# Performance work log

Hardware: AMD Instinct MI355X
Metric: run time of the kernel (lower is better)

The kernel has to match this reference:

```python
import jax, jax.numpy as jnp
import numpy as np

TEMP = 20.0
ATT_WT = 0.5
EPS = 1e-12


def _l2n(x, axis):
    return x / jnp.maximum(jnp.linalg.norm(x, axis=axis, keepdims=True), EPS)


def _conv2d(x, w, b, pad, dil):
    y = jax.lax.conv_general_dilated(
        x, w, window_strides=(1, 1), padding=[(pad, pad), (pad, pad)],
        rhs_dilation=(dil, dil), dimension_numbers=("NCHW", "OIHW", "NCHW"))
    return y + b[None, :, None, None]


def _maxpool3(x):
    return jax.lax.reduce_window(x, -jnp.inf, jax.lax.max,
                                 (1, 1, 3, 3), (1, 1, 3, 3), "VALID")


def setup_inputs() -> dict:
    key = jax.random.key(0)
    ks = jax.random.split(key, 8)
    L, B, C, h, w = 9, 4, 512, 32, 32
    sc = 0.05
    return {
        "fq_feats": jax.random.normal(ks[0], (L, B, C, h, w), jnp.float32),
        "fs_feats": jax.random.normal(ks[1], (L, B, C, h, w), jnp.float32),
        "f_q": jax.random.normal(ks[2], (B, C, h, w), jnp.float32),
        "f_s": jax.random.normal(ks[3], (B, C, h, w), jnp.float32),
        "w1": jax.random.normal(ks[4], (256, 1024, 3, 3), jnp.float32) * sc,
        "b1": jnp.zeros((256,), jnp.float32),
        "w2": jax.random.normal(ks[5], (256, 256, 3, 3), jnp.float32) * sc,
        "b2": jnp.zeros((256,), jnp.float32),
        "w3": jax.random.normal(ks[6], (1, 256, 3, 3), jnp.float32) * sc,
        "b3": jnp.zeros((1,), jnp.float32),
    }


def reference(fq_feats, fs_feats, f_q, f_s, w1, b1, w2, b2, w3, b3):
    B, C, h, w = f_q.shape
    # per-level cosine correlation volumes: normalize over channel dim
    fq_n = _l2n(fq_feats, axis=2)  # [L,B,C,h,w]
    fs_n = _l2n(fs_feats, axis=2)
    corr = jnp.einsum("lbcxy,lbcuv->lbxyuv", fq_n, fs_n)  # [L,B,h,w,h,w]
    # MatchNet corr_forward: ReLU'd volumes fused across hyperpixel levels,
    # temperature softmax over support positions, aggregate support values v=f_s
    corr = jax.nn.relu(corr).mean(axis=0)                 # [B,h,w,h,w]
    attn = jax.nn.softmax(corr.reshape(B, h * w, h * w) * TEMP, axis=-1)
    att_fq = jnp.einsum("bqs,bcs->bcq", attn, f_s.reshape(B, C, h * w))
    att_fq = att_fq.reshape(B, C, h, w)
    fq = _l2n(f_q, axis=1) + _l2n(att_fq, axis=1) * ATT_WT
    # AttentionBranch (Dropout2d is identity at inference)
    comp = jnp.concatenate((f_q, f_s), axis=1)            # [B,1024,h,w]
    x = jax.nn.relu(_conv2d(comp, w1, b1, pad=2, dil=2))  # [B,256,32,32]
    x = _conv2d(x, w2, b2, pad=0, dil=1)                  # [B,256,30,30]
    x = _maxpool3(x)                                      # [B,256,10,10]
    x = _conv2d(x, w3, b3, pad=0, dil=1)                  # [B,1,8,8]
    weight = x.mean(axis=(2, 3)).squeeze()[None]          # [1,B]
    return fq, att_fq, weight
```

## Files before the change

kernel.cpp:

```cpp
#include <hip/hip_runtime.h>
#include <hip/hip_bf16.h>

#define DI __device__ __forceinline__

typedef short bf16x8_t __attribute__((ext_vector_type(8)));
typedef _Float16 f16x8_t __attribute__((ext_vector_type(8)));
typedef float f32x4_t __attribute__((ext_vector_type(4)));

DI unsigned short f2bf(float f) {
    unsigned u = __float_as_uint(f);
    u += 0x7fffu + ((u >> 16) & 1u);
    return (unsigned short)(u >> 16);
}
DI float bfu2f(unsigned short u) { return __uint_as_float(((unsigned)u) << 16); }
DI unsigned short f2h(float f) {
    _Float16 h = (_Float16)f;
    unsigned short u;
    __builtin_memcpy(&u, &h, 2);
    return u;
}
DI float h2f(unsigned short u) {
    _Float16 h;
    __builtin_memcpy(&h, &u, 2);
    return (float)h;
}

__global__ __launch_bounds__(256) void k_prep(const float* __restrict__ fqf,
                                              const float* __restrict__ fsf,
                                              unsigned short* __restrict__ fqb,
                                              unsigned short* __restrict__ fsb,
                                              float* __restrict__ rq,
                                              float* __restrict__ rs) {
    __shared__ float T[128 * 33];
    const int pt = blockIdx.x;
    const int lb = blockIdx.y;
    const int tz = blockIdx.z;
    const float* src = (tz ? fsf : fqf) + (size_t)lb * 524288 + pt * 128;
    unsigned short* dst = (tz ? fsb : fqb) + (((size_t)(lb * 8 + pt)) << 16);
    float* rdst = (tz ? rs : rq) + lb * 1024 + pt * 128;
    const int t = threadIdx.x;

    const int m0 = t >> 2, m1 = 64 + (t >> 2);
    const int q0 = (t & 3) ^ ((m0 >> 2) & 3);
    const int q1 = (t & 3) ^ ((m1 >> 2) & 3);
    float ssq0 = 0.f, ssq1 = 0.f;

    const int brow = t >> 5;
    float4 v[4];
    auto load = [&](int ks) {
#pragma unroll
        for (int j = 0; j < 4; ++j) {
            int f = t + (j << 8);
            int row = f >> 5;
            int m4 = (f & 31) << 2;
            v[j] = *(const float4*)(src + (((size_t)(ks * 32 + row)) << 10) + m4);
        }
    };

    load(0);
    for (int ks = 0; ks < 16; ++ks) {
        __syncthreads();
#pragma unroll
        for (int j = 0; j < 4; ++j) {
            int f = t + (j << 8);
            int row = f >> 5;
            int m4 = (f & 31) << 2;
            T[(m4 + 0) * 33 + row] = v[j].x;
            T[(m4 + 1) * 33 + row] = v[j].y;
            T[(m4 + 2) * 33 + row] = v[j].z;
            T[(m4 + 3) * 33 + row] = v[j].w;
        }
        __syncthreads();
        if (ks < 15) load(ks + 1);
        {
            const float* Tp = &T[m0 * 33 + q0 * 8];
            float f0 = Tp[0], f1 = Tp[1], f2 = Tp[2], f3 = Tp[3];
            float f4 = Tp[4], f5 = Tp[5], f6 = Tp[6], f7 = Tp[7];
            ssq0 += f0 * f0 + f1 * f1 + f2 * f2 + f3 * f3 +
                    f4 * f4 + f5 * f5 + f6 * f6 + f7 * f7;
            uint4 r4;
            r4.x = (unsigned)f2h(f0) | ((unsigned)f2h(f1) << 16);
            r4.y = (unsigned)f2h(f2) | ((unsigned)f2h(f3) << 16);
            r4.z = (unsigned)f2h(f4) | ((unsigned)f2h(f5) << 16);
            r4.w = (unsigned)f2h(f6) | ((unsigned)f2h(f7) << 16);
            *(uint4*)(dst + ((size_t)ks << 12) + ((size_t)t << 3)) = r4;
        }
        {
            const float* Tp = &T[m1 * 33 + q1 * 8];
            float f0 = Tp[0], f1 = Tp[1], f2 = Tp[2], f3 = Tp[3];
            float f4 = Tp[4], f5 = Tp[5], f6 = Tp[6], f7 = Tp[7];
            ssq1 += f0 * f0 + f1 * f1 + f2 * f2 + f3 * f3 +
                    f4 * f4 + f5 * f5 + f6 * f6 + f7 * f7;
            uint4 r4;
            r4.x = (unsigned)f2h(f0) | ((unsigned)f2h(f1) << 16);
            r4.y = (unsigned)f2h(f2) | ((unsigned)f2h(f3) << 16);
            r4.z = (unsigned)f2h(f4) | ((unsigned)f2h(f5) << 16);
            r4.w = (unsigned)f2h(f6) | ((unsigned)f2h(f7) << 16);
            *(uint4*)(dst + ((size_t)ks << 12) + ((size_t)(t + 256) << 3)) = r4;
        }
    }
    ssq0 += __shfl_xor(ssq0, 1); ssq0 += __shfl_xor(ssq0, 2);
    ssq1 += __shfl_xor(ssq1, 1); ssq1 += __shfl_xor(ssq1, 2);
    if ((t & 3) == 0) {
        rdst[m0] = 1.f / fmaxf(sqrtf(ssq0), 1e-12f);
        rdst[m1] = 1.f / fmaxf(sqrtf(ssq1), 1e-12f);
    }
}

__global__ __launch_bounds__(256) void k_corr2(const unsigned short* __restrict__ fqb,
                                               const unsigned short* __restrict__ fsb,
                                               const float* __restrict__ rq,
                                               const float* __restrict__ rs,
                                               unsigned short* __restrict__ P01) {
    __shared__ __align__(16) char L[2][16384];
    const int id = blockIdx.x;
    const int z = id & 7, local = id >> 3;
    const int b = z >> 1, lg = z & 1;
    const int qt = local >> 3, st = local & 7;
    const int q0 = qt * 128, s0 = st * 128;
    const int t = threadIdx.x;
    const int w = t >> 6, lane = t & 63;
    const int wrow = w >> 1, wcol = w & 1;
    const int quad = lane >> 4, m16 = lane & 15;
    const int nsteps = (5 - lg) << 4;

    f32x4_t zero4 = {0.f, 0.f, 0.f, 0.f};
    f32x4_t master[4][4], lvl[4][4];
#pragma unroll
    for (int i = 0; i < 4; ++i)
#pragma unroll
        for (int j = 0; j < 4; ++j) { master[i][j] = zero4; lvl[i][j] = zero4; }

    auto stage = [&](int step, int buf) {
        int g = step >> 4, ks = step & 15;
        int lb = (lg + 2 * g) * 4 + b;
        const unsigned short* Ab = fqb + ((((size_t)lb * 8 + qt) * 16 + ks) << 12);
        const unsigned short* Bb = fsb + ((((size_t)lb * 8 + st) * 16 + ks) << 12);
#pragma unroll
        for (int i = 0; i < 4; ++i) {
            int idx0 = i * 256 + w * 64;
            int idx = idx0 + lane;
            const unsigned short* srcp = (idx0 < 512)
                ? (Ab + ((size_t)idx << 3))
                : (Bb + ((size_t)(idx - 512) << 3));
            __builtin_amdgcn_global_load_lds(
                (const __attribute__((address_space(1))) void*)srcp,
                (__attribute__((address_space(3))) void*)(&L[buf][0] + idx0 * 16),
                16, 0, 0);
        }
    };

    stage(0, 0);
    for (int step = 0; step < nsteps; ++step) {
        const int buf = step & 1;
        __syncthreads();
        if (step < nsteps - 1) stage(step + 1, buf ^ 1);
        const char* base = &L[buf][0];
        f16x8_t af[4], bfr[4];
#pragma unroll
        for (int i = 0; i < 4; ++i) {
            int m = wrow * 64 + i * 16 + m16;
            int sa = quad ^ ((m >> 2) & 3);
            af[i] = *(const f16x8_t*)(base + m * 64 + sa * 16);
            int n = wcol * 64 + i * 16 + m16;
            int sb = quad ^ ((n >> 2) & 3);
            bfr[i] = *(const f16x8_t*)(base + 8192 + n * 64 + sb * 16);
        }
#pragma unroll
        for (int mi = 0; mi < 4; ++mi)
#pragma unroll
            for (int ni = 0; ni < 4; ++ni)
                lvl[mi][ni] = __builtin_amdgcn_mfma_f32_16x16x32_f16(
                    af[mi], bfr[ni], lvl[mi][ni], 0, 0, 0);

        if ((step & 15) == 15) {
            int lb = (lg + 2 * (step >> 4)) * 4 + b;
            const float* rqb = rq + lb * 1024 + q0 + wrow * 64;
            const float* rsb = rs + lb * 1024 + s0 + wcol * 64;
            float rq4[4][4], rsv[4];
#pragma unroll
            for (int mi = 0; mi < 4; ++mi) {
                float4 vv = *(const float4*)(rqb + mi * 16 + quad * 4);
                rq4[mi][0] = vv.x; rq4[mi][1] = vv.y; rq4[mi][2] = vv.z; rq4[mi][3] = vv.w;
            }
#pragma unroll
            for (int ni = 0; ni < 4; ++ni) rsv[ni] = rsb[ni * 16 + m16];
#pragma unroll
            for (int mi = 0; mi < 4; ++mi)
#pragma unroll
                for (int ni = 0; ni < 4; ++ni) {
#pragma unroll
                    for (int e = 0; e < 4; ++e)
                        master[mi][ni][e] += fmaxf(lvl[mi][ni][e] * rq4[mi][e] * rsv[ni], 0.f);
                    lvl[mi][ni] = zero4;
                }
        }
    }

#pragma unroll
    for (int mi = 0; mi < 4; ++mi)
#pragma unroll
        for (int e = 0; e < 4; ++e) {
            int q = q0 + wrow * 64 + mi * 16 + quad * 4 + e;
            unsigned short* cp = P01 + ((((size_t)(lg * 4 + b)) * 1024 + q) << 10)
                                 + s0 + wcol * 64 + m16;
#pragma unroll
            for (int ni = 0; ni < 4; ++ni)
                cp[ni * 16] = f2h(master[mi][ni][e]);
        }
}

__global__ __launch_bounds__(256) void k_softmax(const unsigned short* __restrict__ P01,
                                                 unsigned short* __restrict__ attn) {
    __shared__ float red[8];
    const int row = blockIdx.x;
    const int b = row >> 10, q = row & 1023;
    const int t = threadIdx.x;
    const unsigned short* p0 = P01 + (((size_t)b << 20) + ((size_t)q << 10)) + t * 4;
    const unsigned short* p1 = p0 + ((size_t)4 << 20);
    uint2 a0 = *(const uint2*)p0;
    uint2 a1 = *(const uint2*)p1;
    const float SC = 20.f / 9.f;
    float v0 = (h2f(a0.x & 0xffff) + h2f(a1.x & 0xffff)) * SC;
    float v1 = (h2f(a0.x >> 16)    + h2f(a1.x >> 16)) * SC;
    float v2 = (h2f(a0.y & 0xffff) + h2f(a1.y & 0xffff)) * SC;
    float v3 = (h2f(a0.y >> 16)    + h2f(a1.y >> 16)) * SC;
    float m = fmaxf(fmaxf(v0, v1), fmaxf(v2, v3));
#pragma unroll
    for (int off = 32; off >= 1; off >>= 1) m = fmaxf(m, __shfl_down(m, off));
    const int wid = t >> 6, lane = t & 63;
    if (lane == 0) red[wid] = m;
    __syncthreads();
    m = fmaxf(fmaxf(red[0], red[1]), fmaxf(red[2], red[3]));
    float e0 = __expf(v0 - m), e1 = __expf(v1 - m);
    float e2 = __expf(v2 - m), e3 = __expf(v3 - m);
    float s = e0 + e1 + e2 + e3;
#pragma unroll
    for (int off = 32; off >= 1; off >>= 1) s += __shfl_down(s, off);
    if (lane == 0) red[4 + wid] = s;
    __syncthreads();
    s = red[4] + red[5] + red[6] + red[7];
    float inv = 1.f / s;
    unsigned short* o = attn + (size_t)((b * 32 + (t >> 3)) * 1024 + q) * 36 + (t & 7) * 4;
    uint2 r;
    r.x = (unsigned)f2h(e0 * inv) | ((unsigned)f2h(e1 * inv) << 16);
    r.y = (unsigned)f2h(e2 * inv) | ((unsigned)f2h(e3 * inv) << 16);
    *(uint2*)o = r;
}

__global__ __launch_bounds__(256) void k_fspack(const float* __restrict__ fsi,
                                                unsigned short* __restrict__ fsp) {
    int id = blockIdx.x * 256 + threadIdx.x;
    int c = id & 511, sb = (id >> 9) & 31, b = id >> 14;
    const float4* src = (const float4*)(fsi + (((size_t)(b * 512 + c)) << 10) + sb * 32);
    unsigned short* dst = fsp + (size_t)((b * 32 + sb) * 512 + c) * 36;
#pragma unroll
    for (int j = 0; j < 8; ++j) {
        float4 v = src[j];
        uint2 r;
        r.x = (unsigned)f2h(v.x) | ((unsigned)f2h(v.y) << 16);
        r.y = (unsigned)f2h(v.z) | ((unsigned)f2h(v.w) << 16);
        *(uint2*)(dst + j * 4) = r;
    }
}

__global__ __launch_bounds__(256) void k_attfqm(const unsigned short* __restrict__ fsp,
                                                const unsigned short* __restrict__ attn,
                                                float* __restrict__ attfq) {
    __shared__ __align__(16) char L[2][14336];
    const int q0 = blockIdx.x * 128;
    const int c0 = blockIdx.y * 64;
    const int b  = blockIdx.z;
    const int t = threadIdx.x;
    const int w = t >> 6, lane = t & 63;
    const int quad = lane >> 4, m16 = lane & 15;

    f32x4_t acc[4][2];
#pragma unroll
    for (int i = 0; i < 4; ++i)
#pragma unroll
        for (int j = 0; j < 2; ++j) acc[i][j] = (f32x4_t){0.f, 0.f, 0.f, 0.f};

    auto stage = [&](int sb, int buf) {
        const char* sa = (const char*)(fsp + (size_t)((b * 32 + sb) * 512 + c0) * 36);
        const char* sbp = (const char*)(attn + (size_t)((b * 32 + sb) * 1024 + q0) * 36);
#pragma unroll
        for (int i = 0; i < 4; ++i) {
            int idx0 = i * 256 + w * 64;
            if (idx0 < 896) {
                int idx = idx0 + lane;
                const char* src = (idx < 288) ? (sa + idx * 16) : (sbp + (idx - 288) * 16);
                __builtin_amdgcn_global_load_lds(
                    (const __attribute__((address_space(1))) void*)src,
                    (__attribute__((address_space(3))) void*)(&L[buf][0] + idx0 * 16),
                    16, 0, 0);
            }
        }
    };

    stage(0, 0);
    for (int sb = 0; sb < 32; ++sb) {
        const int buf = sb & 1;
        __syncthreads();
        if (sb < 31) stage(sb + 1, buf ^ 1);
        const char* base = &L[buf][0];
        f16x8_t af[4], bfr[2];
#pragma unroll
        for (int i = 0; i < 4; ++i) {
            const char* ap = base + (size_t)(i * 16 + m16) * 72 + quad * 16;
            union { unsigned long long d[2]; f16x8_t v; } u;
            u.d[0] = *(const unsigned long long*)ap;
            u.d[1] = *(const unsigned long long*)(ap + 8);
            af[i] = u.v;
        }
#pragma unroll
        for (int ni = 0; ni < 2; ++ni) {
            const char* bp = base + 4608 + (size_t)(w * 32 + ni * 16 + m16) * 72 + quad * 16;
            union { unsigned long long d[2]; f16x8_t v; } u;
            u.d[0] = *(const unsigned long long*)bp;
            u.d[1] = *(const unsigned long long*)(bp + 8);
            bfr[ni] = u.v;
        }
#pragma unroll
        for (int mi = 0; mi < 4; ++mi)
#pragma unroll
            for (int ni = 0; ni < 2; ++ni)
                acc[mi][ni] = __builtin_amdgcn_mfma_f32_16x16x32_f16(
                    af[mi], bfr[ni], acc[mi][ni], 0, 0, 0);
    }

#pragma unroll
    for (int mi = 0; mi < 4; ++mi)
#pragma unroll
        for (int e = 0; e < 4; ++e) {
            int c = c0 + mi * 16 + quad * 4 + e;
            float* rowp = attfq + (((size_t)(b * 512 + c)) << 10) + q0 + w * 32 + m16;
#pragma unroll
            for (int ni = 0; ni < 2; ++ni)
                rowp[ni * 16] = acc[mi][ni][e];
        }
}

__global__ __launch_bounds__(256) void k_out(const float* __restrict__ fqi,
                                             const float* __restrict__ attfq,
                                             float* __restrict__ out) {
    __shared__ float redq[256], reda[256];
    __shared__ float rnq[64], rna[64];
    const int b = blockIdx.y;
    const int p0 = blockIdx.x * 64;
    const int t = threadIdx.x;
    const int pl = t & 63, cg = t >> 6;
    const int pos = p0 + pl;
    const float* qp = fqi + (((size_t)b) << 19) + pos;
    const float* ap = attfq + (((size_t)b) << 19) + pos;
    float sq = 0.f, sa = 0.f;
    for (int c = cg * 128; c < cg * 128 + 128; ++c) {
        float q = qp[(size_t)c << 10];
        float a = ap[(size_t)c << 10];
        sq += q * q;
        sa += a * a;
    }
    redq[t] = sq; reda[t] = sa;
    __syncthreads();
    if (t < 64) {
        float q = redq[t] + redq[t + 64] + redq[t + 128] + redq[t + 192];
        float a = reda[t] + reda[t + 64] + reda[t + 128] + reda[t + 192];
        rnq[t] = 1.f / fmaxf(sqrtf(q), 1e-12f);
        rna[t] = 1.f / fmaxf(sqrtf(a), 1e-12f);
    }
    __syncthreads();
    const float RQ = rnq[pl], RA = 0.5f * rna[pl];
    float* o1 = out + (((size_t)b) << 19) + pos;
    float* o2 = o1 + 2097152;
    for (int c = cg * 128; c < cg * 128 + 128; ++c) {
        float q = qp[(size_t)c << 10];
        float a = ap[(size_t)c << 10];
        o1[(size_t)c << 10] = q * RQ + a * RA;
        o2[(size_t)c << 10] = a;
    }
}

__global__ __launch_bounds__(256) void k_w1pack(const float* __restrict__ w1,
                                                unsigned short* __restrict__ w1p) {
    int pid = blockIdx.x * 256 + threadIdx.x;
    int oc = pid >> 10, ic = pid & 1023;
    const float* src = w1 + (size_t)pid * 9;
    float f[9];
#pragma unroll
    for (int tp = 0; tp < 9; ++tp) f[tp] = src[tp];
    int s = ic >> 5, j = ic & 31;
#pragma unroll
    for (int tp = 0; tp < 9; ++tp) {
        size_t row = ((size_t)(tp * 32 + s) * 256 + oc) * 40;
        w1p[row + j] = f2bf(f[tp]);
        if (j < 8) w1p[row + 32 + j] = 0;
    }
}

__global__ __launch_bounds__(256) void k_conv1m(const float* __restrict__ fqi,
                                                const float* __restrict__ fsi,
                                                const unsigned short* __restrict__ w1p,
                                                float* __restrict__ P) {
    __shared__ __align__(16) char As[2][20480];
    __shared__ __align__(16) char Bs[2][4096];
    const int p0 = blockIdx.x * 64;
    const int b = blockIdx.y;
    const int tap = blockIdx.z;
    const int dy = 2 * (tap / 3) - 2;
    const int dx = 2 * (tap % 3) - 2;
    const int t = threadIdx.x;
    const int w = t >> 6, lane = t & 63;
    const int quad = lane >> 4, m16 = lane & 15;
    const int bn = t & 63, kg = t >> 6;
    const int e0 = p0 + bn;
    const bool valid = ((unsigned)((e0 >> 5) + dy) < 32u) &&
                       ((unsigned)((e0 & 31) + dx) < 32u);
    const int cidx = min(max(e0 + dy * 32 + dx, 0), 1023);
    const int bchunk = (bn * 4 + (kg ^ (bn & 3))) * 16;

    f32x4_t acc[4][4];
#pragma unroll
    for (int i = 0; i < 4; ++i)
#pragma unroll
        for (int j = 0; j < 4; ++j) acc[i][j] = (f32x4_t){0.f, 0.f, 0.f, 0.f};

    auto stageA = [&](int s, int buf) {
        const char* src = (const char*)(w1p + (size_t)(tap * 32 + s) * 10240);
#pragma unroll
        for (int i = 0; i < 5; ++i) {
            int idx = i * 4 + w;
            __builtin_amdgcn_global_load_lds(
                (const __attribute__((address_space(1))) void*)(src + idx * 1024 + lane * 16),
                (__attribute__((address_space(3))) void*)(&As[buf][0] + idx * 1024),
                16, 0, 0);
        }
    };
    auto stageB = [&](int s, int buf) {
        int ch = s * 32 + kg * 8;
        const float* plane = (ch < 512)
            ? (fqi + (((size_t)(b * 512 + ch)) << 10))
            : (fsi + (((size_t)(b * 512 + ch - 512)) << 10));
        float f[8];
#pragma unroll
        for (int j = 0; j < 8; ++j) {
            float v = plane[((size_t)j << 10) + cidx];
            f[j] = valid ? v : 0.f;
        }
        uint4 r4;
        r4.x = (unsigned)f2bf(f[0]) | ((unsigned)f2bf(f[1]) << 16);
        r4.y = (unsigned)f2bf(f[2]) | ((unsigned)f2bf(f[3]) << 16);
        r4.z = (unsigned)f2bf(f[4]) | ((unsigned)f2bf(f[5]) << 16);
        r4.w = (unsigned)f2bf(f[6]) | ((unsigned)f2bf(f[7]) << 16);
        *(uint4*)(&Bs[buf][bchunk]) = r4;
    };

    stageA(0, 0);
    stageB(0, 0);

    for (int s = 0; s < 32; ++s) {
        const int buf = s & 1;
        __syncthreads();
        if (s < 31) {
            stageA(s + 1, buf ^ 1);
            stageB(s + 1, buf ^ 1);
        }
        bf16x8_t af[4], bfr[4];
#pragma unroll
        for (int i = 0; i < 4; ++i) {
            af[i] = *(const bf16x8_t*)(&As[buf][0] + (size_t)(w * 64 + i * 16 + m16) * 80 + quad * 16);
            int nn = i * 16 + m16;
            bfr[i] = *(const bf16x8_t*)(&Bs[buf][0] + (nn * 4 + (quad ^ (nn & 3))) * 16);
        }
#pragma unroll
        for (int mi = 0; mi < 4; ++mi)
#pragma unroll
            for (int ni = 0; ni < 4; ++ni)
                acc[mi][ni] = __builtin_amdgcn_mfma_f32_16x16x32_bf16(
                    af[mi], bfr[ni], acc[mi][ni], 0, 0, 0);
    }

    float* Pb = P + (((size_t)(tap * 4 + b)) << 18) + p0;
#pragma unroll
    for (int mi = 0; mi < 4; ++mi)
#pragma unroll
        for (int e = 0; e < 4; ++e) {
            int oc = w * 64 + mi * 16 + quad * 4 + e;
            float* row = Pb + (size_t)oc * 1024 + m16;
#pragma unroll
            for (int ni = 0; ni < 4; ++ni)
                row[ni * 16] = acc[mi][ni][e];
        }
}

__global__ __launch_bounds__(256) void k_c1comb(const float* __restrict__ P,
                                                const float* __restrict__ b1,
                                                unsigned short* __restrict__ x1) {
    int id = blockIdx.x * 256 + threadIdx.x;
    int oc = (id >> 8) & 255;
    const float4* P4 = (const float4*)P;
    float bb = b1[oc];
    float4 a = P4[id];
    a.x += bb; a.y += bb; a.z += bb; a.w += bb;
#pragma unroll
    for (int tp = 1; tp < 9; ++tp) {
        float4 v = P4[id + tp * 262144];
        a.x += v.x; a.y += v.y; a.z += v.z; a.w += v.w;
    }
    float o0 = fmaxf(a.x, 0.f);
    float o1 = fmaxf(a.y, 0.f);
    float o2 = fmaxf(a.z, 0.f);
    float o3 = fmaxf(a.w, 0.f);
    uint2 r;
    r.x = (unsigned)f2bf(o0) | ((unsigned)f2bf(o1) << 16);
    r.y = (unsigned)f2bf(o2) | ((unsigned)f2bf(o3) << 16);
    ((uint2*)x1)[id] = r;
}

__global__ __launch_bounds__(256) void k_w2pack(const float* __restrict__ w2,
                                                unsigned short* __restrict__ w2p) {
    int pid = blockIdx.x * 256 + threadIdx.x;
    int oc = pid >> 8, ic = pid & 255;
    const float* src = w2 + (size_t)pid * 9;
    float f[9];
#pragma unroll
    for (int tp = 0; tp < 9; ++tp) f[tp] = src[tp];
    int s = ic >> 5, j = ic & 31;
#pragma unroll
    for (int tp = 0; tp < 9; ++tp) {
        size_t row = ((size_t)(tp * 8 + s) * 256 + oc) * 40;
        w2p[row + j] = f2bf(f[tp]);
        if (j < 8) w2p[row + 32 + j] = 0;
    }
}

__global__ __launch_bounds__(256) void k_conv2m(const unsigned short* __restrict__ x1,
                                                const unsigned short* __restrict__ w2p,
                                                float* __restrict__ P2) {
    __shared__ __align__(16) char As[2][20480];
    __shared__ __align__(16) char Bs[2][4096];
    const int p0 = blockIdx.x * 64;
    const int b = blockIdx.y;
    const int tap = blockIdx.z;
    const int t = threadIdx.x;
    const int w = t >> 6, lane = t & 63;
    const int quad = lane >> 4, m16 = lane & 15;
    const int bn = t & 63, kg = t >> 6;
    const int e0 = p0 + bn;
    const int cidx = min(e0 + (tap / 3) * 32 + (tap % 3), 1023);
    const int bchunk = (bn * 4 + (kg ^ (bn & 3))) * 16;

    f32x4_t acc[4][4];
#pragma unroll
    for (int i = 0; i < 4; ++i)
#pragma unroll
        for (int j = 0; j < 4; ++j) acc[i][j] = (f32x4_t){0.f, 0.f, 0.f, 0.f};

    auto stageA = [&](int s, int buf) {
        const char* src = (const char*)(w2p + (size_t)(tap * 8 + s) * 10240);
#pragma unroll
        for (int i = 0; i < 5; ++i) {
            int idx = i * 4 + w;
            __builtin_amdgcn_global_load_lds(
                (const __attribute__((address_space(1))) void*)(src + idx * 1024 + lane * 16),
                (__attribute__((address_space(3))) void*)(&As[buf][0] + idx * 1024),
                16, 0, 0);
        }
    };
    auto stageB = [&](int s, int buf) {
        int ch = s * 32 + kg * 8;
        const unsigned short* plane = x1 + (((size_t)(b * 256 + ch)) << 10);
        unsigned short u[8];
#pragma unroll
        for (int j = 0; j < 8; ++j) u[j] = plane[((size_t)j << 10) + cidx];
        uint4 r4;
        r4.x = (unsigned)u[0] | ((unsigned)u[1] << 16);
        r4.y = (unsigned)u[2] | ((unsigned)u[3] << 16);
        r4.z = (unsigned)u[4] | ((unsigned)u[5] << 16);
        r4.w = (unsigned)u[6] | ((unsigned)u[7] << 16);
        *(uint4*)(&Bs[buf][bchunk]) = r4;
    };

    stageA(0, 0);
    stageB(0, 0);

    for (int s = 0; s < 8; ++s) {
        const int buf = s & 1;
        __syncthreads();
        if (s < 7) {
            stageA(s + 1, buf ^ 1);
            stageB(s + 1, buf ^ 1);
        }
        bf16x8_t af[4], bfr[4];
#pragma unroll
        for (int i = 0; i < 4; ++i) {
            af[i] = *(const bf16x8_t*)(&As[buf][0] + (size_t)(w * 64 + i * 16 + m16) * 80 + quad * 16);
            int nn = i * 16 + m16;
            bfr[i] = *(const bf16x8_t*)(&Bs[buf][0] + (nn * 4 + (quad ^ (nn & 3))) * 16);
        }
#pragma unroll
        for (int mi = 0; mi < 4; ++mi)
#pragma unroll
            for (int ni = 0; ni < 4; ++ni)
                acc[mi][ni] = __builtin_amdgcn_mfma_f32_16x16x32_bf16(
                    af[mi], bfr[ni], acc[mi][ni], 0, 0, 0);
    }

    float* Pb = P2 + (((size_t)(tap * 4 + b)) << 18) + p0;
#pragma unroll
    for (int mi = 0; mi < 4; ++mi)
#pragma unroll
        for (int e = 0; e < 4; ++e) {
            int oc = w * 64 + mi * 16 + quad * 4 + e;
            float* row = Pb + (size_t)oc * 1024 + m16;
#pragma unroll
            for (int ni = 0; ni < 4; ++ni)
                row[ni * 16] = acc[mi][ni][e];
        }
}

__global__ __launch_bounds__(256) void k_c2pool(const float* __restrict__ P2,
                                                const float* __restrict__ b2,
                                                float* __restrict__ xp) {
    int id = blockIdx.x * 256 + threadIdx.x;
    int px = id % 10;
    int tmp = id / 10;
    int py = tmp % 10;
    int ch = tmp / 10;
    int b = ch >> 8, oc = ch & 255;
    float bb = b2[oc];
    float m = -3.4e38f;
#pragma unroll
    for (int dy = 0; dy < 3; ++dy)
#pragma unroll
        for (int dx = 0; dx < 3; ++dx) {
            int pos = (3 * py + dy) * 32 + 3 * px + dx;
            float v = bb;
#pragma unroll
            for (int tp = 0; tp < 9; ++tp)
                v += P2[(((size_t)(tp * 4 + b)) << 18) + (size_t)oc * 1024 + pos];
            m = fmaxf(m, v);
        }
    xp[id] = m;
}

__global__ __launch_bounds__(256) void k_conv3(const float* __restrict__ xp,
                                               const float* __restrict__ w3,
                                               const float* __restrict__ b3,
                                               float* __restrict__ out) {
    __shared__ float s[256];
    int b = blockIdx.x, t = threadIdx.x;
    int pos = t & 63, qi = t >> 6;
    int y = pos >> 3, x = pos & 7;
    float acc = 0.f;
    for (int ic = qi * 64; ic < qi * 64 + 64; ++ic) {
        const float* ip = xp + ((size_t)(b * 256 + ic)) * 100 + y * 10 + x;
#pragma unroll
        for (int kh = 0; kh < 3; ++kh)
#pragma unroll
            for (int kw = 0; kw < 3; ++kw)
                acc = fmaf(w3[ic * 9 + kh * 3 + kw], ip[kh * 10 + kw], acc);
    }
    s[t] = acc;
    __syncthreads();
    if (t < 64) {
        float v = s[t] + s[t + 64] + s[t + 128] + s[t + 192];
#pragma unroll
        for (int off = 32; off >= 1; off >>= 1) v += __shfl_down(v, off);
        if (t == 0) out[4194304 + b] = v * (1.f / 64.f) + b3[0];
    }
}

extern "C" void kernel_launch(void* const* d_in, const int* in_sizes, int n_in,
                              void* d_out, int out_size, void* d_ws, size_t ws_size,
                              hipStream_t stream) {
    (void)in_sizes; (void)n_in; (void)out_size; (void)ws_size;
    const float* fqf = (const float*)d_in[0];
    const float* fsf = (const float*)d_in[1];
    const float* fqi = (const float*)d_in[2];
    const float* fsi = (const float*)d_in[3];
    const float* w1  = (const float*)d_in[4];
    const float* b1  = (const float*)d_in[5];
    const float* w2  = (const float*)d_in[6];
    const float* b2  = (const float*)d_in[7];
    const float* w3  = (const float*)d_in[8];
    const float* b3  = (const float*)d_in[9];
    float* out = (float*)d_out;

    float* W = (float*)d_ws;
    unsigned short* P01u = (unsigned short*)W;
    float* attfq = W;
    unsigned short* attn = (unsigned short*)(W + 4194304);
    unsigned short* w1p  = (unsigned short*)(W + 4194304);
    float* rq = W + 5668864;
    float* rs = W + 5705728;
    unsigned short* w2p  = (unsigned short*)(W + 4194304);
    unsigned short* fsp = (unsigned short*)(W + 6553600);
    unsigned short* x1 = (unsigned short*)(W + 7733248);
    float* xp = W + 8257536;
    unsigned short* fqb = (unsigned short*)(W + 8359936);
    float* P9 = W + 8359936;
    unsigned short* fsb = (unsigned short*)(W + 17797120);

    hipLaunchKernelGGL(k_w1pack,  dim3(1024),      dim3(256), 0, stream, w1, w1p);
    hipLaunchKernelGGL(k_conv1m,  dim3(16, 4, 9),  dim3(256), 0, stream, fqi, fsi, w1p, P9);
    hipLaunchKernelGGL(k_c1comb,  dim3(1024),      dim3(256), 0, stream, P9, b1, x1);
    hipLaunchKernelGGL(k_fspack,  dim3(256),       dim3(256), 0, stream, fsi, fsp);
    hipLaunchKernelGGL(k_prep,    dim3(8, 36, 2),  dim3(256), 0, stream, fqf, fsf, fqb, fsb, rq, rs);
    hipLaunchKernelGGL(k_corr2,   dim3(512),       dim3(256), 0, stream, fqb, fsb, rq, rs, P01u);
    hipLaunchKernelGGL(k_softmax, dim3(4096),      dim3(256), 0, stream, P01u, attn);
    hipLaunchKernelGGL(k_attfqm,  dim3(8, 8, 4),   dim3(256), 0, stream, fsp, attn, attfq);
    hipLaunchKernelGGL(k_out,     dim3(16, 4),     dim3(256), 0, stream, fqi, attfq, out);
    hipLaunchKernelGGL(k_w2pack,  dim3(256),       dim3(256), 0, stream, w2, w2p);
    hipLaunchKernelGGL(k_conv2m,  dim3(16, 4, 9),  dim3(256), 0, stream, x1, w2p, P9);
    hipLaunchKernelGGL(k_c2pool,  dim3(400),       dim3(256), 0, stream, P9, b2, xp);
    hipLaunchKernelGGL(k_conv3,   dim3(4),         dim3(256), 0, stream, xp, w3, b3, out);
}
```

Baseline: 450.9 us.

## Split prep over channel groups with partial norms, double-buffer LDS, widen k_out grid

k_prep now splits the 512-channel reduction into four groups per block, which quadruples the grid. Each group writes partial sums of squares, and a new k_rfold kernel combines them into reciprocal norms. The transpose tile in LDS is double-buffered, so one barrier per step covers both the write and the read. k_out uses 16 positions per block instead of 64, giving a 4x larger grid. This adds parallelism to the memory-bound kernels at the cost of one extra launch and less coalescing in k_out, since only 16 contiguous floats are read per row.

```diff
diff --git a/kernel.cpp b/kernel.cpp
--- a/kernel.cpp
+++ b/kernel.cpp
@@ -29,15 +29,16 @@
                                               const float* __restrict__ fsf,
                                               unsigned short* __restrict__ fqb,
                                               unsigned short* __restrict__ fsb,
-                                              float* __restrict__ rq,
-                                              float* __restrict__ rs) {
-    __shared__ float T[128 * 33];
+                                              float* __restrict__ rpart) {
+    __shared__ float T[2][128 * 33];
     const int pt = blockIdx.x;
     const int lb = blockIdx.y;
-    const int tz = blockIdx.z;
+    const int zz = blockIdx.z;
+    const int tz = zz >> 2, kg = zz & 3;
+    const int ks0 = kg * 4;
     const float* src = (tz ? fsf : fqf) + (size_t)lb * 524288 + pt * 128;
     unsigned short* dst = (tz ? fsb : fqb) + (((size_t)(lb * 8 + pt)) << 16);
-    float* rdst = (tz ? rs : rq) + lb * 1024 + pt * 128;
+    float* rdst = rpart + (size_t)tz * 147456 + (size_t)kg * 36864 + lb * 1024 + pt * 128;
     const int t = threadIdx.x;
 
     const int m0 = t >> 2, m1 = 64 + (t >> 2);
@@ -45,7 +46,6 @@
     const int q1 = (t & 3) ^ ((m1 >> 2) & 3);
     float ssq0 = 0.f, ssq1 = 0.f;
 
-    const int brow = t >> 5;
     float4 v[4];
     auto load = [&](int ks) {
 #pragma unroll
@@ -56,24 +56,29 @@
             v[j] = *(const float4*)(src + (((size_t)(ks * 32 + row)) << 10) + m4);
         }
     };
-
-    load(0);
-    for (int ks = 0; ks < 16; ++ks) {
-        __syncthreads();
+    auto writeT = [&](int buf) {
 #pragma unroll
         for (int j = 0; j < 4; ++j) {
             int f = t + (j << 8);
             int row = f >> 5;
             int m4 = (f & 31) << 2;
-            T[(m4 + 0) * 33 + row] = v[j].x;
-            T[(m4 + 1) * 33 + row] = v[j].y;
-            T[(m4 + 2) * 33 + row] = v[j].z;
-            T[(m4 + 3) * 33 + row] = v[j].w;
-        }
+            float* Tb = &T[buf][0];
+            Tb[(m4 + 0) * 33 + row] = v[j].x;
+            Tb[(m4 + 1) * 33 + row] = v[j].y;
+            Tb[(m4 + 2) * 33 + row] = v[j].z;
+            Tb[(m4 + 3) * 33 + row] = v[j].w;
+        }
+    };
+
+    load(ks0);
+    writeT(0);
+    for (int s = 0; s < 4; ++s) {
         __syncthreads();
-        if (ks < 15) load(ks + 1);
+        if (s < 3) load(ks0 + s + 1);
+        const int ks = ks0 + s;
+        const float* Tb = &T[s & 1][0];
         {
-            const float* Tp = &T[m0 * 33 + q0 * 8];
+            const float* Tp = Tb + m0 * 33 + q0 * 8;
             float f0 = Tp[0], f1 = Tp[1], f2 = Tp[2], f3 = Tp[3];
             float f4 = Tp[4], f5 = Tp[5], f6 = Tp[6], f7 = Tp[7];
             ssq0 += f0 * f0 + f1 * f1 + f2 * f2 + f3 * f3 +
@@ -86,7 +91,7 @@
             *(uint4*)(dst + ((size_t)ks << 12) + ((size_t)t << 3)) = r4;
         }
         {
-            const float* Tp = &T[m1 * 33 + q1 * 8];
+            const float* Tp = Tb + m1 * 33 + q1 * 8;
             float f0 = Tp[0], f1 = Tp[1], f2 = Tp[2], f3 = Tp[3];
             float f4 = Tp[4], f5 = Tp[5], f6 = Tp[6], f7 = Tp[7];
             ssq1 += f0 * f0 + f1 * f1 + f2 * f2 + f3 * f3 +
@@ -98,13 +103,24 @@
             r4.w = (unsigned)f2h(f6) | ((unsigned)f2h(f7) << 16);
             *(uint4*)(dst + ((size_t)ks << 12) + ((size_t)(t + 256) << 3)) = r4;
         }
+        if (s < 3) writeT((s + 1) & 1);
     }
     ssq0 += __shfl_xor(ssq0, 1); ssq0 += __shfl_xor(ssq0, 2);
     ssq1 += __shfl_xor(ssq1, 1); ssq1 += __shfl_xor(ssq1, 2);
     if ((t & 3) == 0) {
-        rdst[m0] = 1.f / fmaxf(sqrtf(ssq0), 1e-12f);
-        rdst[m1] = 1.f / fmaxf(sqrtf(ssq1), 1e-12f);
-    }
+        rdst[m0] = ssq0;
+        rdst[m1] = ssq1;
+    }
+}
+
+__global__ __launch_bounds__(256) void k_rfold(const float* __restrict__ rpart,
+                                               float* __restrict__ rout) {
+    int id = blockIdx.x * 256 + threadIdx.x;
+    int tz = id >= 36864;
+    int i = id - (tz ? 36864 : 0);
+    const float* p = rpart + (size_t)tz * 147456 + i;
+    float s = p[0] + p[36864] + p[73728] + p[110592];
+    rout[id] = 1.f / fmaxf(sqrtf(s), 1e-12f);
 }
 
 __global__ __launch_bounds__(256) void k_corr2(const unsigned short* __restrict__ fqb,
@@ -345,16 +361,16 @@
                                              const float* __restrict__ attfq,
                                              float* __restrict__ out) {
     __shared__ float redq[256], reda[256];
-    __shared__ float rnq[64], rna[64];
+    __shared__ float rnq[16], rna[16];
     const int b = blockIdx.y;
-    const int p0 = blockIdx.x * 64;
+    const int p0 = blockIdx.x * 16;
     const int t = threadIdx.x;
-    const int pl = t & 63, cg = t >> 6;
+    const int pl = t & 15, cg = t >> 4;
     const int pos = p0 + pl;
     const float* qp = fqi + (((size_t)b) << 19) + pos;
     const float* ap = attfq + (((size_t)b) << 19) + pos;
     float sq = 0.f, sa = 0.f;
-    for (int c = cg * 128; c < cg * 128 + 128; ++c) {
+    for (int c = cg * 32; c < cg * 32 + 32; ++c) {
         float q = qp[(size_t)c << 10];
         float a = ap[(size_t)c << 10];
         sq += q * q;
@@ -362,17 +378,18 @@
     }
     redq[t] = sq; reda[t] = sa;
     __syncthreads();
-    if (t < 64) {
-        float q = redq[t] + redq[t + 64] + redq[t + 128] + redq[t + 192];
-        float a = reda[t] + reda[t + 64] + reda[t + 128] + reda[t + 192];
+    if (t < 16) {
+        float q = 0.f, a = 0.f;
+#pragma unroll
+        for (int j = 0; j < 16; ++j) { q += redq[t + j * 16]; a += reda[t + j * 16]; }
         rnq[t] = 1.f / fmaxf(sqrtf(q), 1e-12f);
-        rna[t] = 1.f / fmaxf(sqrtf(a), 1e-12f);
+        rna[t] = 0.5f / fmaxf(sqrtf(a), 1e-12f);
     }
     __syncthreads();
-    const float RQ = rnq[pl], RA = 0.5f * rna[pl];
+    const float RQ = rnq[pl], RA = rna[pl];
     float* o1 = out + (((size_t)b) << 19) + pos;
     float* o2 = o1 + 2097152;
-    for (int c = cg * 128; c < cg * 128 + 128; ++c) {
+    for (int c = cg * 32; c < cg * 32 + 32; ++c) {
         float q = qp[(size_t)c << 10];
         float a = ap[(size_t)c << 10];
         o1[(size_t)c << 10] = q * RQ + a * RA;
@@ -691,8 +708,9 @@
     float* attfq = W;
     unsigned short* attn = (unsigned short*)(W + 4194304);
     unsigned short* w1p  = (unsigned short*)(W + 4194304);
-    float* rq = W + 5668864;
-    float* rs = W + 5705728;
+    float* rpart = W + 5668864;
+    float* rq = W + 5963776;
+    float* rs = W + 6000640;
     unsigned short* w2p  = (unsigned short*)(W + 4194304);
     unsigned short* fsp = (unsigned short*)(W + 6553600);
     unsigned short* x1 = (unsigned short*)(W + 7733248);
@@ -705,11 +723,12 @@
     hipLaunchKernelGGL(k_conv1m,  dim3(16, 4, 9),  dim3(256), 0, stream, fqi, fsi, w1p, P9);
     hipLaunchKernelGGL(k_c1comb,  dim3(1024),      dim3(256), 0, stream, P9, b1, x1);
     hipLaunchKernelGGL(k_fspack,  dim3(256),       dim3(256), 0, stream, fsi, fsp);
-    hipLaunchKernelGGL(k_prep,    dim3(8, 36, 2),  dim3(256), 0, stream, fqf, fsf, fqb, fsb, rq, rs);
+    hipLaunchKernelGGL(k_prep,    dim3(8, 36, 8),  dim3(256), 0, stream, fqf, fsf, fqb, fsb, rpart);
+    hipLaunchKernelGGL(k_rfold,   dim3(288),       dim3(256), 0, stream, rpart, rq);
     hipLaunchKernelGGL(k_corr2,   dim3(512),       dim3(256), 0, stream, fqb, fsb, rq, rs, P01u);
     hipLaunchKernelGGL(k_softmax, dim3(4096),      dim3(256), 0, stream, P01u, attn);
     hipLaunchKernelGGL(k_attfqm,  dim3(8, 8, 4),   dim3(256), 0, stream, fsp, attn, attfq);
-    hipLaunchKernelGGL(k_out,     dim3(16, 4),     dim3(256), 0, stream, fqi, attfq, out);
+    hipLaunchKernelGGL(k_out,     dim3(64, 4),     dim3(256), 0, stream, fqi, attfq, out);
     hipLaunchKernelGGL(k_w2pack,  dim3(256),       dim3(256), 0, stream, w2, w2p);
     hipLaunchKernelGGL(k_conv2m,  dim3(16, 4, 9),  dim3(256), 0, stream, x1, w2p, P9);
     hipLaunchKernelGGL(k_c2pool,  dim3(400),       dim3(256), 0, stream, P9, b2, xp);
```

New measurement: 423.0 us. -6.2%, faster.
